# Kernel optimization log

Measured on AMD Instinct MI355X. Metric: run time of the kernel, lower is better.

The kernel has to match this reference:

```python
import jax, jax.numpy as jnp
import numpy as np

D_MODEL = 1024
N_HEADS = 16
D_HEAD = D_MODEL // N_HEADS  # 64
NUM_MEM_KV = 4
SCALE = D_HEAD ** -0.5


def setup_inputs() -> dict:
    key = jax.random.key(0)
    k1, k2, k3, k4 = jax.random.split(key, 4)
    x = jax.random.normal(k1, (4, 4096, D_MODEL), dtype=jnp.float32)
    mask = jax.random.randint(k2, (4, 4096), 0, 2).astype(jnp.int32)
    w_qkv = jax.random.normal(k3, (3 * D_MODEL, D_MODEL), dtype=jnp.float32) * 0.02
    mem_kv = jax.random.normal(k4, (2, N_HEADS, NUM_MEM_KV, D_HEAD), dtype=jnp.float32)
    return {"x": x, "w_qkv": w_qkv, "mem_kv": mem_kv, "mask": mask}


def reference(x, w_qkv, mem_kv, mask):
    b, l, _ = x.shape
    # qkv projection: nn.Linear applies x @ W^T; reshape matches torch view(..., h, d_head, 3)
    qkv = jnp.einsum('bld,ed->ble', x, w_qkv).reshape(b, l, N_HEADS, D_HEAD, 3)
    qkv = jnp.moveaxis(qkv, 2, 1)  # (b, h, l, d_head, 3)
    q, k, v = qkv[..., 0], qkv[..., 1], qkv[..., 2]

    m = mask.astype(x.dtype)[:, None, :, None]  # (b, 1, l, 1) per prepare_mask
    k = jnp.where(m == 0, -jnp.inf, k * m)

    # prepend learned memory kv along the sequence axis
    mk = jnp.broadcast_to(mem_kv[0], (b, N_HEADS, NUM_MEM_KV, D_HEAD))
    mv = jnp.broadcast_to(mem_kv[1], (b, N_HEADS, NUM_MEM_KV, D_HEAD))
    k = jnp.concatenate([mk, k], axis=-2)  # (b, h, m+l, d_head)
    v = jnp.concatenate([mv, v], axis=-2)

    q = jax.nn.softmax(q * SCALE, axis=-1)   # softmax over feature dim
    k = jax.nn.softmax(k, axis=-2)           # softmax over sequence dim; -inf rows -> 0 weight

    context = jnp.einsum('bhnd,bhne->bhde', k, v)   # (b, h, d_head, d_head)
    out = jnp.einsum('bhld,bhde->bhle', q, context)  # (b, h, l, d_head)
    out = out * m
    out = jnp.moveaxis(out, 1, 2).reshape(b, l, N_HEADS * D_HEAD)
    return out
```

## Files before the change

kernel.cpp:

```cpp
#include <hip/hip_runtime.h>

typedef _Float16 h8 __attribute__((ext_vector_type(8)));
typedef _Float16 h4 __attribute__((ext_vector_type(4)));
typedef float f4 __attribute__((ext_vector_type(4)));

typedef __attribute__((address_space(1))) const void GV;
typedef __attribute__((address_space(3))) void SV;

__device__ __forceinline__ void async16(const void* g, void* s) {
  __builtin_amdgcn_global_load_lds((GV*)g, (SV*)s, 16, 0, 0);
}


#define XC 2097152

__global__ __launch_bounds__(256) void cvt_f16(const float4* __restrict__ x,
                                               const float4* __restrict__ w,
                                               h8* __restrict__ xh,
                                               h8* __restrict__ wh) {
  int t = blockIdx.x * 256 + threadIdx.x;
  if (t < XC) {
    const int row = t >> 7, c7 = t & 127;
    const int dst = (row << 7) | (c7 & 120) | ((c7 & 7) ^ (row & 7));
    float4 a = x[t * 2], b = x[t * 2 + 1];
    h8 o = {(_Float16)a.x, (_Float16)a.y, (_Float16)a.z, (_Float16)a.w,
            (_Float16)b.x, (_Float16)b.y, (_Float16)b.z, (_Float16)b.w};
    xh[dst] = o;
  } else {
    const int u = t - XC;
    const int rp = u >> 7, c7 = u & 127;
    int sr;
    if (rp < 2048) {
      int h = rp >> 7, c = rp & 127;
      sr = h * 192 + ((c < 64) ? (c * 3 + 1) : ((c - 64) * 3 + 2));
    } else {
      int q = rp - 2048;
      sr = (q >> 6) * 192 + (q & 63) * 3;
    }
    const int dst = (rp << 7) | (c7 & 120) | ((c7 & 7) ^ (rp & 7));
    float4 a = w[sr * 256 + c7 * 2], b = w[sr * 256 + c7 * 2 + 1];
    h8 o = {(_Float16)a.x, (_Float16)a.y, (_Float16)a.z, (_Float16)a.w,
            (_Float16)b.x, (_Float16)b.y, (_Float16)b.z, (_Float16)b.w};
    wh[dst] = o;
  }
}

__global__ __launch_bounds__(256, 3) void kv_gemm(const _Float16* __restrict__ A,
                                                  const _Float16* __restrict__ W,
                                                  const int* __restrict__ mask,
                                                  float* __restrict__ part) {
  __shared__ _Float16 smem[128 * 128];
  _Float16* const As = smem;
  _Float16* const Bs = smem + 8192;
  const int tid = threadIdx.x;
  const int lane = tid & 63, wid = tid >> 6;
  const int wm = wid & 1, wn = wid >> 1;
  const int l15 = lane & 15, quad = lane >> 4;
  const int m0 = blockIdx.y * 128;
  const int n0 = blockIdx.x * 128;

  const f4 z = {0.f, 0.f, 0.f, 0.f};
  f4 acc[4][4];
#pragma unroll
  for (int i = 0; i < 4; ++i)
#pragma unroll
    for (int j = 0; j < 4; ++j) acc[i][j] = z;

  const int swz = l15 & 7;

  for (int kt = 0; kt < 16; ++kt) {
    const int k0 = kt * 64;
#pragma unroll
    for (int it = 0; it < 4; ++it) {
      const int idx = it * 256 + tid;
      const int row = idx >> 3, cg = idx & 7;
      async16(A + ((size_t)(m0 + row) * 1024 + k0 + cg * 8), As + idx * 8);
      async16(W + ((size_t)(n0 + row) * 1024 + k0 + cg * 8), Bs + idx * 8);
    }
    __syncthreads();
#pragma unroll
    for (int ks = 0; ks < 2; ++ks) {
      const int pc = ((ks << 2) | quad) ^ swz;
      h8 af[4], bf[4];
#pragma unroll
      for (int i = 0; i < 4; ++i)
        af[i] = *(const h8*)&As[(wm * 64 + i * 16 + l15) * 64 + pc * 8];
#pragma unroll
      for (int j = 0; j < 4; ++j)
        bf[j] = *(const h8*)&Bs[(wn * 64 + j * 16 + l15) * 64 + pc * 8];
#pragma unroll
      for (int i = 0; i < 4; ++i)
#pragma unroll
        for (int j = 0; j < 4; ++j)
          acc[i][j] = __builtin_amdgcn_mfma_f32_16x16x32_f16(af[i], bf[j], acc[i][j], 0, 0, 0);
    }
    __syncthreads();
  }

  const int h = n0 >> 7;
  const int b = m0 >> 12;
  const int lc = (m0 & 4095) >> 7;
  const int bh = b * 16 + h;
#pragma unroll
  for (int i = 0; i < 4; ++i) {
    const int nb = wm * 64 + i * 16 + quad * 4;
#pragma unroll
    for (int j = 0; j < 4; ++j) {
      const int c = wn * 64 + j * 16 + l15;
      h4 o;
      if (wn == 0) {
#pragma unroll
        for (int r = 0; r < 4; ++r)
          o[r] = (_Float16)(mask[m0 + nb + r] ? __expf(acc[i][j][r]) : 0.f);
      } else {
#pragma unroll
        for (int r = 0; r < 4; ++r) o[r] = (_Float16)acc[i][j][r];
      }
      *(h4*)&smem[c * 128 + (nb ^ (l15 * 8))] = o;
    }
  }
  __syncthreads();
  f4 cacc[5];
#pragma unroll
  for (int i = 0; i < 5; ++i) cacc[i] = z;
  h8 bones;
  {
    const _Float16 o1 = (l15 == 0) ? (_Float16)1.f : (_Float16)0.f;
#pragma unroll
    for (int j = 0; j < 8; ++j) bones[j] = o1;
  }
  const int ds = wid * 16;
#pragma unroll
  for (int ks = 0; ks < 4; ++ks) {
    const int nb2 = (ks * 32 + quad * 8) ^ (l15 * 8);
    h8 a = *(const h8*)&smem[(ds + l15) * 128 + nb2];
#pragma unroll
    for (int et = 0; et < 4; ++et) {
      h8 bv = *(const h8*)&smem[(64 + et * 16 + l15) * 128 + nb2];
      cacc[et] = __builtin_amdgcn_mfma_f32_16x16x32_f16(a, bv, cacc[et], 0, 0, 0);
    }
    cacc[4] = __builtin_amdgcn_mfma_f32_16x16x32_f16(a, bones, cacc[4], 0, 0, 0);
  }
  const size_t pb = ((size_t)bh * 32 + lc) * 4160;
  const int dw = ds + quad * 4;
#pragma unroll
  for (int et = 0; et < 4; ++et)
#pragma unroll
    for (int r = 0; r < 4; ++r)
      part[pb + (size_t)(dw + r) * 64 + et * 16 + l15] = cacc[et][r];
  if (l15 == 0) {
#pragma unroll
    for (int r = 0; r < 4; ++r) part[pb + 4096 + dw + r] = cacc[4][r];
  }
}

__global__ __launch_bounds__(256) void reduce_ctx(const float* __restrict__ part,
                                                  const float* __restrict__ memkv,
                                                  _Float16* __restrict__ ctxt) {
  const int bh = blockIdx.x;
  const int dsl = blockIdx.y;
  const int h = bh & 15;
  const int tid = threadIdx.x;
  const int dl = tid >> 6, e = tid & 63;
  const int d = dsl * 4 + dl;
  const size_t pb = (size_t)bh * 32 * 4160;

  float den = 0.f;
#pragma unroll 8
  for (int c = 0; c < 32; ++c) den += part[pb + (size_t)c * 4160 + 4096 + d];
  float s = 0.f;
#pragma unroll 8
  for (int c = 0; c < 32; ++c) s += part[pb + (size_t)c * 4160 + (size_t)d * 64 + e];
#pragma unroll
  for (int j = 0; j < 4; ++j) {
    const float ek = __expf(memkv[(h * 4 + j) * 64 + d]);
    den += ek;
    s += ek * memkv[4096 + (h * 4 + j) * 64 + e];
  }
  ctxt[(size_t)bh * 4096 + (size_t)e * 64 + d] = (_Float16)(s / den);
}

__global__ __launch_bounds__(256, 3) void qpv(const _Float16* __restrict__ A,
                                              const _Float16* __restrict__ W,
                                              const _Float16* __restrict__ ctxt,
                                              const int* __restrict__ mask,
                                              float* __restrict__ out) {
  __shared__ _Float16 smem[128 * 128];
  _Float16* const As = smem;
  _Float16* const Bs = smem + 8192;
  const int tid = threadIdx.x;
  const int lane = tid & 63, wid = tid >> 6;
  const int wm = wid & 1, wn = wid >> 1;
  const int l15 = lane & 15, quad = lane >> 4;
  const int m0 = blockIdx.y * 128;
  const int n0 = blockIdx.x * 128;

  const f4 z = {0.f, 0.f, 0.f, 0.f};
  f4 acc[4][4];
#pragma unroll
  for (int i = 0; i < 4; ++i)
#pragma unroll
    for (int j = 0; j < 4; ++j) acc[i][j] = z;

  const int swz = l15 & 7;

  for (int kt = 0; kt < 16; ++kt) {
    const int k0 = kt * 64;
#pragma unroll
    for (int it = 0; it < 4; ++it) {
      const int idx = it * 256 + tid;
      const int row = idx >> 3, cg = idx & 7;
      async16(A + ((size_t)(m0 + row) * 1024 + k0 + cg * 8), As + idx * 8);
      async16(W + ((size_t)(2048 + n0 + row) * 1024 + k0 + cg * 8), Bs + idx * 8);
    }
    __syncthreads();
#pragma unroll
    for (int ks = 0; ks < 2; ++ks) {
      const int pc = ((ks << 2) | quad) ^ swz;
      h8 af[4], bf[4];
#pragma unroll
      for (int i = 0; i < 4; ++i)
        af[i] = *(const h8*)&As[(wm * 64 + i * 16 + l15) * 64 + pc * 8];
#pragma unroll
      for (int j = 0; j < 4; ++j)
        bf[j] = *(const h8*)&Bs[(wn * 64 + j * 16 + l15) * 64 + pc * 8];
#pragma unroll
      for (int i = 0; i < 4; ++i)
#pragma unroll
        for (int j = 0; j < 4; ++j)
          acc[i][j] = __builtin_amdgcn_mfma_f32_16x16x32_f16(bf[j], af[i], acc[i][j], 0, 0, 0);
    }
    __syncthreads();
  }

#pragma unroll
  for (int i = 0; i < 4; ++i) {
    const int m = wm * 64 + i * 16 + l15;
    _Float16* const prow = &smem[m * 128 + wn * 64];
#pragma unroll
    for (int j = 0; j < 4; ++j) {
      h4 o;
#pragma unroll
      for (int r = 0; r < 4; ++r) o[r] = (_Float16)__expf(acc[i][j][r] * 0.125f);
      const int c3 = (j * 2 + (quad >> 1)) ^ (l15 & 7);
      *(h4*)&prow[c3 * 8 + (quad & 1) * 4] = o;
    }
  }
  __syncthreads();

  const int hw = wid >> 1;
  const int mb = (wid & 1) * 64;
  const int h = (n0 >> 6) + hw;
  const int bh = (m0 >> 12) * 16 + h;
  f4 cacc[4][5];
#pragma unroll
  for (int i = 0; i < 4; ++i)
#pragma unroll
    for (int j = 0; j < 5; ++j) cacc[i][j] = z;
  h8 bones;
  {
    const _Float16 o1 = (l15 == 0) ? (_Float16)1.f : (_Float16)0.f;
#pragma unroll
    for (int j = 0; j < 8; ++j) bones[j] = o1;
  }
#pragma unroll
  for (int ks = 0; ks < 2; ++ks) {
    h8 bf[4];
#pragma unroll
    for (int et = 0; et < 4; ++et)
      bf[et] = *(const h8*)&ctxt[(size_t)bh * 4096 +
                                 (size_t)(et * 16 + l15) * 64 + ks * 32 + quad * 8];
#pragma unroll
    for (int i2 = 0; i2 < 4; ++i2) {
      const int m = mb + i2 * 16 + l15;
      const int ch = ((ks * 4 + quad) ^ (l15 & 7)) * 8;
      h8 a = *(const h8*)&smem[m * 128 + hw * 64 + ch];
#pragma unroll
      for (int et = 0; et < 4; ++et)
        cacc[i2][et] = __builtin_amdgcn_mfma_f32_16x16x32_f16(a, bf[et], cacc[i2][et], 0, 0, 0);
      cacc[i2][4] = __builtin_amdgcn_mfma_f32_16x16x32_f16(a, bones, cacc[i2][4], 0, 0, 0);
    }
  }
#pragma unroll
  for (int i2 = 0; i2 < 4; ++i2) {
#pragma unroll
    for (int r = 0; r < 4; ++r) {
      const int row = m0 + mb + i2 * 16 + quad * 4 + r;
      const float sb = __shfl(cacc[i2][4][r], lane & 48);
      const float iv = mask[row] ? 1.0f / sb : 0.0f;
#pragma unroll
      for (int et = 0; et < 4; ++et)
        out[(size_t)row * 1024 + h * 64 + et * 16 + l15] = cacc[i2][et][r] * iv;
    }
  }
}

extern "C" void kernel_launch(void* const* d_in, const int* in_sizes, int n_in,
                              void* d_out, int out_size, void* d_ws, size_t ws_size,
                              hipStream_t stream) {
  const float* x = (const float*)d_in[0];
  const float* w = (const float*)d_in[1];
  const float* memkv = (const float*)d_in[2];
  const int* mask = (const int*)d_in[3];
  float* out = (float*)d_out;

  char* ws = (char*)d_ws;
  _Float16* xh   = (_Float16*)(ws + 0);
  _Float16* wh   = (_Float16*)(ws + 33554432);
  float*    part = (float*)(ws + 39845888);
  _Float16* ctxt = (_Float16*)(ws + 73924608);

  cvt_f16<<<dim3(9728), dim3(256), 0, stream>>>((const float4*)x, (const float4*)w,
                                                (h8*)xh, (h8*)wh);
  kv_gemm<<<dim3(16, 128), dim3(256), 0, stream>>>(xh, wh, mask, part);
  reduce_ctx<<<dim3(64, 16), dim3(256), 0, stream>>>(part, memkv, ctxt);
  qpv<<<dim3(8, 128), dim3(256), 0, stream>>>(xh, wh, ctxt, mask, out);
}
```

Before: 262.0 us.

## Compact masked rows and skip GEMM tiles for masked-out sequence positions

Adds a compaction kernel that builds per-batch lists of unmasked row indices using atomics. The kv and q GEMMs gather only the unmasked rows, return early for tiles past the valid count, and scatter outputs back. Masked output rows are zeroed inside the conversion kernel. This removes GEMM work on masked rows, which is about half the rows for random masks, at the cost of gathered loads, an extra memset plus compaction launch, and a larger conversion grid.

```diff
diff --git a/kernel.cpp b/kernel.cpp
--- a/kernel.cpp
+++ b/kernel.cpp
@@ -13,11 +13,29 @@
 
 
 #define XC 2097152
+#define WC 393216
+#define ZC 4194304
+
+__global__ __launch_bounds__(256) void compact(const int* __restrict__ mask,
+                                               int* __restrict__ cnt,
+                                               int* __restrict__ idx) {
+  const int n = blockIdx.x * 256 + threadIdx.x;
+  const int b = n >> 12, r = n & 4095;
+  if (mask[n]) {
+    const int p = atomicAdd(&cnt[b], 1);
+    idx[b * 4096 + p] = r;
+  } else {
+    const int p = atomicAdd(&cnt[b + 4], 1);
+    idx[b * 4096 + 4095 - p] = r;
+  }
+}
 
 __global__ __launch_bounds__(256) void cvt_f16(const float4* __restrict__ x,
                                                const float4* __restrict__ w,
+                                               const int* __restrict__ mask,
                                                h8* __restrict__ xh,
-                                               h8* __restrict__ wh) {
+                                               h8* __restrict__ wh,
+                                               float4* __restrict__ out) {
   int t = blockIdx.x * 256 + threadIdx.x;
   if (t < XC) {
     const int row = t >> 7, c7 = t & 127;
@@ -26,7 +44,7 @@
     h8 o = {(_Float16)a.x, (_Float16)a.y, (_Float16)a.z, (_Float16)a.w,
             (_Float16)b.x, (_Float16)b.y, (_Float16)b.z, (_Float16)b.w};
     xh[dst] = o;
-  } else {
+  } else if (t < XC + WC) {
     const int u = t - XC;
     const int rp = u >> 7, c7 = u & 127;
     int sr;
@@ -42,13 +60,26 @@
     h8 o = {(_Float16)a.x, (_Float16)a.y, (_Float16)a.z, (_Float16)a.w,
             (_Float16)b.x, (_Float16)b.y, (_Float16)b.z, (_Float16)b.w};
     wh[dst] = o;
+  } else {
+    const int u = t - (XC + WC);
+    const int row = u >> 8, c = u & 255;
+    if (!mask[row]) {
+      const float4 z4 = {0.f, 0.f, 0.f, 0.f};
+      out[(size_t)row * 256 + c] = z4;
+    }
   }
 }
 
 __global__ __launch_bounds__(256, 3) void kv_gemm(const _Float16* __restrict__ A,
                                                   const _Float16* __restrict__ W,
-                                                  const int* __restrict__ mask,
+                                                  const int* __restrict__ cnt,
+                                                  const int* __restrict__ idx,
                                                   float* __restrict__ part) {
+  const int my = blockIdx.y;
+  const int b = my >> 5, lc = my & 31;
+  const int cb = cnt[b];
+  if (lc * 128 >= cb) return;
+
   __shared__ _Float16 smem[128 * 128];
   _Float16* const As = smem;
   _Float16* const Bs = smem + 8192;
@@ -56,8 +87,17 @@
   const int lane = tid & 63, wid = tid >> 6;
   const int wm = wid & 1, wn = wid >> 1;
   const int l15 = lane & 15, quad = lane >> 4;
-  const int m0 = blockIdx.y * 128;
   const int n0 = blockIdx.x * 128;
+
+  int rsrc[4], x7[4];
+#pragma unroll
+  for (int it = 0; it < 4; ++it) {
+    const int s = it * 32 + (tid >> 3);
+    const int ri = idx[b * 4096 + lc * 128 + s];
+    rsrc[it] = b * 4096 + ri;
+    x7[it] = (s & 7) ^ (ri & 7);
+  }
+  const int cg = tid & 7;
 
   const f4 z = {0.f, 0.f, 0.f, 0.f};
   f4 acc[4][4];
@@ -72,10 +112,10 @@
     const int k0 = kt * 64;
 #pragma unroll
     for (int it = 0; it < 4; ++it) {
-      const int idx = it * 256 + tid;
-      const int row = idx >> 3, cg = idx & 7;
-      async16(A + ((size_t)(m0 + row) * 1024 + k0 + cg * 8), As + idx * 8);
-      async16(W + ((size_t)(n0 + row) * 1024 + k0 + cg * 8), Bs + idx * 8);
+      const int idxl = it * 256 + tid;
+      const int brow = idxl >> 3;
+      async16(A + ((size_t)rsrc[it] * 1024 + k0 + (cg ^ x7[it]) * 8), As + idxl * 8);
+      async16(W + ((size_t)(n0 + brow) * 1024 + k0 + cg * 8), Bs + idxl * 8);
     }
     __syncthreads();
 #pragma unroll
@@ -98,9 +138,8 @@
   }
 
   const int h = n0 >> 7;
-  const int b = m0 >> 12;
-  const int lc = (m0 & 4095) >> 7;
   const int bh = b * 16 + h;
+  const int jbase = lc * 128;
 #pragma unroll
   for (int i = 0; i < 4; ++i) {
     const int nb = wm * 64 + i * 16 + quad * 4;
@@ -111,7 +150,7 @@
       if (wn == 0) {
 #pragma unroll
         for (int r = 0; r < 4; ++r)
-          o[r] = (_Float16)(mask[m0 + nb + r] ? __expf(acc[i][j][r]) : 0.f);
+          o[r] = (_Float16)((jbase + nb + r < cb) ? __expf(acc[i][j][r]) : 0.f);
       } else {
 #pragma unroll
         for (int r = 0; r < 4; ++r) o[r] = (_Float16)acc[i][j][r];
@@ -156,6 +195,7 @@
 
 __global__ __launch_bounds__(256) void reduce_ctx(const float* __restrict__ part,
                                                   const float* __restrict__ memkv,
+                                                  const int* __restrict__ cnt,
                                                   _Float16* __restrict__ ctxt) {
   const int bh = blockIdx.x;
   const int dsl = blockIdx.y;
@@ -164,13 +204,12 @@
   const int dl = tid >> 6, e = tid & 63;
   const int d = dsl * 4 + dl;
   const size_t pb = (size_t)bh * 32 * 4160;
+  const int nch = (cnt[bh >> 4] + 127) >> 7;
 
   float den = 0.f;
-#pragma unroll 8
-  for (int c = 0; c < 32; ++c) den += part[pb + (size_t)c * 4160 + 4096 + d];
+  for (int c = 0; c < nch; ++c) den += part[pb + (size_t)c * 4160 + 4096 + d];
   float s = 0.f;
-#pragma unroll 8
-  for (int c = 0; c < 32; ++c) s += part[pb + (size_t)c * 4160 + (size_t)d * 64 + e];
+  for (int c = 0; c < nch; ++c) s += part[pb + (size_t)c * 4160 + (size_t)d * 64 + e];
 #pragma unroll
   for (int j = 0; j < 4; ++j) {
     const float ek = __expf(memkv[(h * 4 + j) * 64 + d]);
@@ -183,8 +222,14 @@
 __global__ __launch_bounds__(256, 3) void qpv(const _Float16* __restrict__ A,
                                               const _Float16* __restrict__ W,
                                               const _Float16* __restrict__ ctxt,
-                                              const int* __restrict__ mask,
+                                              const int* __restrict__ cnt,
+                                              const int* __restrict__ idx,
                                               float* __restrict__ out) {
+  const int my = blockIdx.y;
+  const int b = my >> 5, lc = my & 31;
+  const int cb = cnt[b];
+  if (lc * 128 >= cb) return;
+
   __shared__ _Float16 smem[128 * 128];
   _Float16* const As = smem;
   _Float16* const Bs = smem + 8192;
@@ -192,8 +237,17 @@
   const int lane = tid & 63, wid = tid >> 6;
   const int wm = wid & 1, wn = wid >> 1;
   const int l15 = lane & 15, quad = lane >> 4;
-  const int m0 = blockIdx.y * 128;
   const int n0 = blockIdx.x * 128;
+
+  int rsrc[4], x7[4];
+#pragma unroll
+  for (int it = 0; it < 4; ++it) {
+    const int s = it * 32 + (tid >> 3);
+    const int ri = idx[b * 4096 + lc * 128 + s];
+    rsrc[it] = b * 4096 + ri;
+    x7[it] = (s & 7) ^ (ri & 7);
+  }
+  const int cg = tid & 7;
 
   const f4 z = {0.f, 0.f, 0.f, 0.f};
   f4 acc[4][4];
@@ -208,10 +262,10 @@
     const int k0 = kt * 64;
 #pragma unroll
     for (int it = 0; it < 4; ++it) {
-      const int idx = it * 256 + tid;
-      const int row = idx >> 3, cg = idx & 7;
-      async16(A + ((size_t)(m0 + row) * 1024 + k0 + cg * 8), As + idx * 8);
-      async16(W + ((size_t)(2048 + n0 + row) * 1024 + k0 + cg * 8), Bs + idx * 8);
+      const int idxl = it * 256 + tid;
+      const int brow = idxl >> 3;
+      async16(A + ((size_t)rsrc[it] * 1024 + k0 + (cg ^ x7[it]) * 8), As + idxl * 8);
+      async16(W + ((size_t)(2048 + n0 + brow) * 1024 + k0 + cg * 8), Bs + idxl * 8);
     }
     __syncthreads();
 #pragma unroll
@@ -251,7 +305,7 @@
   const int hw = wid >> 1;
   const int mb = (wid & 1) * 64;
   const int h = (n0 >> 6) + hw;
-  const int bh = (m0 >> 12) * 16 + h;
+  const int bh = b * 16 + h;
   f4 cacc[4][5];
 #pragma unroll
   for (int i = 0; i < 4; ++i)
@@ -285,12 +339,16 @@
   for (int i2 = 0; i2 < 4; ++i2) {
 #pragma unroll
     for (int r = 0; r < 4; ++r) {
-      const int row = m0 + mb + i2 * 16 + quad * 4 + r;
+      const int s = mb + i2 * 16 + quad * 4 + r;
+      const int j = lc * 128 + s;
       const float sb = __shfl(cacc[i2][4][r], lane & 48);
-      const float iv = mask[row] ? 1.0f / sb : 0.0f;
-#pragma unroll
-      for (int et = 0; et < 4; ++et)
-        out[(size_t)row * 1024 + h * 64 + et * 16 + l15] = cacc[i2][et][r] * iv;
+      if (j < cb) {
+        const int row = b * 4096 + idx[b * 4096 + j];
+        const float iv = 1.0f / sb;
+#pragma unroll
+        for (int et = 0; et < 4; ++et)
+          out[(size_t)row * 1024 + h * 64 + et * 16 + l15] = cacc[i2][et][r] * iv;
+      }
     }
   }
 }
@@ -309,10 +367,14 @@
   _Float16* wh   = (_Float16*)(ws + 33554432);
   float*    part = (float*)(ws + 39845888);
   _Float16* ctxt = (_Float16*)(ws + 73924608);
-
-  cvt_f16<<<dim3(9728), dim3(256), 0, stream>>>((const float4*)x, (const float4*)w,
-                                                (h8*)xh, (h8*)wh);
-  kv_gemm<<<dim3(16, 128), dim3(256), 0, stream>>>(xh, wh, mask, part);
-  reduce_ctx<<<dim3(64, 16), dim3(256), 0, stream>>>(part, memkv, ctxt);
-  qpv<<<dim3(8, 128), dim3(256), 0, stream>>>(xh, wh, ctxt, mask, out);
-}
+  int*      cnt  = (int*)(ws + 74448896);
+  int*      idx  = (int*)(ws + 74448928);
+
+  hipMemsetAsync(cnt, 0, 32, stream);
+  compact<<<dim3(64), dim3(256), 0, stream>>>(mask, cnt, idx);
+  cvt_f16<<<dim3(26112), dim3(256), 0, stream>>>((const float4*)x, (const float4*)w,
+                                                 mask, (h8*)xh, (h8*)wh, (float4*)out);
+  kv_gemm<<<dim3(16, 128), dim3(256), 0, stream>>>(xh, wh, cnt, idx, part);
+  reduce_ctx<<<dim3(64, 16), dim3(256), 0, stream>>>(part, memkv, cnt, ctxt);
+  qpv<<<dim3(8, 128), dim3(256), 0, stream>>>(xh, wh, ctxt, cnt, idx, out);
+}
```

Result: slower. 417.7 us (+59.4%).
